# Optimization experiments

Measured on AMD Instinct MI355X. Metric: run time of the kernel, lower is better.

## Reference

```python
import jax, jax.numpy as jnp
import numpy as np

H = 8          # num_heads
D = 64         # head_dim
HID = 512      # hidden_size
W = 128        # window_size
NEG = -1e9

def setup_inputs() -> dict:
    key = jax.random.key(0)
    ks = jax.random.split(key, 12)
    B, S = 2, 2048
    def lin(i):
        w = jax.random.normal(ks[i], (HID, HID), dtype=jnp.float32) * (1.0 / np.sqrt(HID))
        b = jax.random.normal(ks[i + 1], (HID,), dtype=jnp.float32) * 0.01
        return w, b
    Wq, bq = lin(0)
    Wk, bk = lin(2)
    Wv, bv = lin(4)
    Wo, bo = lin(6)
    return {
        "value": jax.random.normal(ks[8], (B, S, HID), dtype=jnp.float32),
        "key": jax.random.normal(ks[9], (B, S, HID), dtype=jnp.float32),
        "query": jax.random.normal(ks[10], (B, S, HID), dtype=jnp.float32),
        "Wq": Wq, "bq": bq, "Wk": Wk, "bk": bk,
        "Wv": Wv, "bv": bv, "Wo": Wo, "bo": bo,
    }

def reference(value, key, query, Wq, bq, Wk, bk, Wv, bv, Wo, bo):
    B, S, _ = query.shape
    def heads(x, Wt, b):
        # torch Linear: x @ W.T + b ; then [B,S,H,D] -> [B,H,S,D]
        return (x @ Wt.T + b).reshape(B, S, H, D).transpose(0, 2, 1, 3)
    Q = heads(query, Wq, bq)
    K = heads(key, Wk, bk)
    V = heads(value, Wv, bv)
    scores = jnp.einsum('bhqd,bhkd->bhqk', Q, K) / jnp.sqrt(jnp.float32(D))
    idx = jnp.arange(S)
    local = jnp.abs(idx[:, None] - idx[None, :]) <= W  # [S,S] band mask
    scores = jnp.where(local[None, None], scores, NEG)
    weights = jax.nn.softmax(scores, axis=-1)
    out = jnp.einsum('bhqk,bhkd->bhqd', weights, V)
    out = out.transpose(0, 2, 1, 3).reshape(B, S, HID)
    return out @ Wo.T + bo
```

## Files before the change

kernel.cpp:

```cpp
#include <hip/hip_runtime.h>
#include <stdint.h>

#define B_   2
#define S_   2048
#define H_   8
#define D_   64
#define HID_ 512
#define W_   128
#define M_   (B_ * S_)
#define E_   (M_ * HID_)
#define WE_  (HID_ * HID_)
#define PPAD_ 72
#define M0_  12.0f

typedef unsigned short u16;
typedef __attribute__((ext_vector_type(8))) __bf16 bf16x8;
typedef __attribute__((ext_vector_type(4))) float  floatx4;

__device__ __forceinline__ float b2f(u16 u) {
    union { unsigned int i; float f; } x;
    x.i = ((unsigned int)u) << 16;
    return x.f;
}
__device__ __forceinline__ u16 f2b(float f) {
    union { float f; unsigned int i; } x;
    x.f = f;
    unsigned int r = x.i + 0x7FFFu + ((x.i >> 16) & 1u);
    return (u16)(r >> 16);
}

__device__ __forceinline__ void gll16(const u16* g, u16* l) {
    __builtin_amdgcn_global_load_lds(
        (const __attribute__((address_space(1))) unsigned int*)g,
        (__attribute__((address_space(3))) unsigned int*)l, 16, 0, 0);
}

__global__ __launch_bounds__(256) void split_kernel(
    const float* __restrict__ q, const float* __restrict__ k, const float* __restrict__ v,
    const float* __restrict__ wq, const float* __restrict__ wk,
    const float* __restrict__ wv, const float* __restrict__ wo,
    u16* __restrict__ U) {
    const int y = blockIdx.y;
    const float* src;
    u16* dst;
    int n;
    if (y < 3) {
        src = (y == 0) ? q : (y == 1) ? k : v;
        dst = U + (size_t)y * E_;
        n = E_;
    } else {
        src = (y == 3) ? wq : (y == 4) ? wk : (y == 5) ? wv : wo;
        dst = U + 3 * (size_t)E_ + (size_t)(y - 3) * WE_;
        n = WE_;
    }
    const int idx = (blockIdx.x * 256 + threadIdx.x) * 4;
    if (idx >= n) return;
    const float4 x = *(const float4*)(src + idx);
    ushort4 hs;
    hs.x = f2b(x.x); hs.y = f2b(x.y); hs.z = f2b(x.z); hs.w = f2b(x.w);
    *(ushort4*)(dst + idx) = hs;
}

template <int MODE, int PASSES, int BM, int BN>
__device__ __forceinline__ void gemm_mfma_body(
    const u16* __restrict__ Xh, const u16* __restrict__ Xl,
    const u16* __restrict__ Wh, const float* __restrict__ bias,
    float* __restrict__ outF, u16* __restrict__ outH) {
    constexpr int TM = BM / 64;
    constexpr int TN = BN / 16;
    constexpr int AGRP = BM / 16;
    constexpr int BGRP = BN / 16;

    __shared__ u16 As[2][PASSES][2][BM * 32];
    __shared__ u16 Bs[2][2][BN * 32];

    const int tid  = threadIdx.x;
    const int wave = tid >> 6;
    const int lane = tid & 63;
    const int r16  = lane & 15;
    const int quad = lane >> 4;
    const int srow = lane >> 2;
    const int sk   = (lane & 3) * 8;
    const int m0 = blockIdx.x * BM;
    const int n0 = blockIdx.y * BN;

    floatx4 zero = {0.f, 0.f, 0.f, 0.f};
    floatx4 acc[TM][TN];
#pragma unroll
    for (int i = 0; i < TM; i++)
#pragma unroll
        for (int j = 0; j < TN; j++) acc[i][j] = zero;

    auto stage = [&](int buf, int k0) {
        int slot = 0;
#pragma unroll
        for (int p = 0; p < PASSES; p++)
#pragma unroll
            for (int ks = 0; ks < 2; ks++)
#pragma unroll
                for (int g = 0; g < AGRP; g++, slot++)
                    if ((slot & 3) == wave) {
                        const u16* src = (p ? Xl : Xh) +
                            (size_t)(m0 + g * 16 + srow) * HID_ + k0 + ks * 32 + sk;
                        gll16(src, &As[buf][p][ks][g * 16 * 32]);
                    }
#pragma unroll
        for (int ks = 0; ks < 2; ks++)
#pragma unroll
            for (int g = 0; g < BGRP; g++, slot++)
                if ((slot & 3) == wave) {
                    const u16* src = Wh +
                        (size_t)(n0 + g * 16 + srow) * HID_ + k0 + ks * 32 + sk;
                    gll16(src, &Bs[buf][ks][g * 16 * 32]);
                }
    };

    stage(0, 0);
    constexpr int NIT = HID_ / 64;
    for (int it = 0; it < NIT; it++) {
        __syncthreads();
        if (it + 1 < NIT) stage((it + 1) & 1, (it + 1) * 64);
        const int buf = it & 1;

        bf16x8 bfr[2][TN];
#pragma unroll
        for (int ks = 0; ks < 2; ks++)
#pragma unroll
            for (int j = 0; j < TN; j++)
                bfr[ks][j] = *(const bf16x8*)&Bs[buf][ks][(j * 16 + r16) * 32 + quad * 8];
#pragma unroll
        for (int p = 0; p < PASSES; p++) {
            bf16x8 afr[2][TM];
#pragma unroll
            for (int ks = 0; ks < 2; ks++)
#pragma unroll
                for (int i = 0; i < TM; i++)
                    afr[ks][i] = *(const bf16x8*)
                        &As[buf][p][ks][(wave * TM * 16 + i * 16 + r16) * 32 + quad * 8];
#pragma unroll
            for (int ks = 0; ks < 2; ks++)
#pragma unroll
                for (int i = 0; i < TM; i++)
#pragma unroll
                    for (int j = 0; j < TN; j++)
                        acc[i][j] = __builtin_amdgcn_mfma_f32_16x16x32_bf16(
                            afr[ks][i], bfr[ks][j], acc[i][j], 0, 0, 0);
        }
    }

    const int m_base = m0 + wave * TM * 16;
    const int bb = m_base >> 11;
    if (MODE == 0) {
#pragma unroll
        for (int j = 0; j < TN; j++) {
            const int col = n0 + j * 16 + r16;
            const float bv = bias[col];
#pragma unroll
            for (int i = 0; i < TM; i++) {
                const int row0 = m_base + i * 16 + quad * 4;
#pragma unroll
                for (int r = 0; r < 4; r++)
                    outF[(size_t)(row0 + r) * HID_ + col] = acc[i][j][r] + bv;
            }
        }
    } else if (MODE == 1) {
#pragma unroll
        for (int j = 0; j < TN; j++) {
            const int col = n0 + j * 16 + r16;
            const int h = col >> 6, d = col & (D_ - 1);
            const float bv = bias[col];
            const size_t base = (size_t)(bb * H_ + h) * S_;
#pragma unroll
            for (int i = 0; i < TM; i++)
#pragma unroll
                for (int r = 0; r < 4; r++) {
                    const int s = (m_base & (S_ - 1)) + i * 16 + quad * 4 + r;
                    outH[(base + s) * D_ + d] = f2b(acc[i][j][r] + bv);
                }
        }
    } else {
#pragma unroll
        for (int j = 0; j < TN; j++) {
            const int col = n0 + j * 16 + r16;
            const int h = col >> 6, d = col & (D_ - 1);
            const float bv = bias[col];
            const size_t base = ((size_t)(bb * H_ + h) * D_ + d) * S_;
            const int s0 = (m_base & (S_ - 1)) + quad * 4;
#pragma unroll
            for (int i = 0; i < TM; i++) {
                ushort4 hs;
                hs.x = f2b(acc[i][j][0] + bv);
                hs.y = f2b(acc[i][j][1] + bv);
                hs.z = f2b(acc[i][j][2] + bv);
                hs.w = f2b(acc[i][j][3] + bv);
                *(ushort4*)(outH + base + s0 + i * 16) = hs;
            }
        }
    }
}

__global__ __launch_bounds__(256) void qkv_mfma_kernel(
    const u16* __restrict__ U,
    const float* __restrict__ bq, const float* __restrict__ bk, const float* __restrict__ bv,
    u16* __restrict__ P) {
    const u16* Wb = U + 3 * (size_t)E_;
    if (blockIdx.z == 0)
        gemm_mfma_body<1, 1, 128, 64>(U, nullptr, Wb, bq, nullptr, P);
    else if (blockIdx.z == 1)
        gemm_mfma_body<1, 1, 128, 64>(U + E_, nullptr, Wb + WE_, bk, nullptr, P + E_);
    else
        gemm_mfma_body<2, 1, 128, 64>(U + 2 * (size_t)E_, nullptr, Wb + 2 * WE_, bv,
                                      nullptr, P + 2 * (size_t)E_);
}

__global__ __launch_bounds__(256) void out_mfma_kernel(
    const u16* __restrict__ AOh, const u16* __restrict__ AOl,
    const u16* __restrict__ Woh, const float* __restrict__ bo,
    float* __restrict__ out) {
    gemm_mfma_body<0, 2, 64, 32>(AOh, AOl, Woh, bo, out, nullptr);
}

__global__ __launch_bounds__(256) void attn_kernel(
    const u16* __restrict__ Qh, const u16* __restrict__ Kh,
    const u16* __restrict__ Vth,
    u16* __restrict__ AOh, u16* __restrict__ AOl) {
    __shared__ u16   Ps[4][64][PPAD_];
    __shared__ float Ored[64][68];
    __shared__ float Lred[4][64];

    const int tid  = threadIdx.x;
    const int wave = tid >> 6;
    const int lane = tid & 63;
    const int r16 = lane & 15, quad = lane >> 4;
    const int qt = blockIdx.x, bh = blockIdx.y;
    const int q0 = qt * 64;
    const size_t sd = (size_t)bh * S_ * D_;
    const size_t ds = (size_t)bh * D_ * S_;

    floatx4 zero = {0.f, 0.f, 0.f, 0.f};
    floatx4 O[4][4];
    float lsum[4][4];
#pragma unroll
    for (int i = 0; i < 4; i++)
#pragma unroll
        for (int j = 0; j < 4; j++) O[i][j] = zero;
#pragma unroll
    for (int i = 0; i < 4; i++)
#pragma unroll
        for (int r = 0; r < 4; r++) lsum[i][r] = 0.f;

    int t_lo = qt - 2; if (t_lo < 0) t_lo = 0;
    int t_hi = qt + 2; if (t_hi > S_ / 64 - 1) t_hi = S_ / 64 - 1;

    for (int t = t_lo + wave; t <= t_hi; t += 4) {
        const int k0 = t * 64;
        floatx4 sa[4][4];
#pragma unroll
        for (int i = 0; i < 4; i++)
#pragma unroll
            for (int j = 0; j < 4; j++) sa[i][j] = zero;

#pragma unroll
        for (int ks = 0; ks < 2; ks++) {
            bf16x8 qf[4], kf[4];
#pragma unroll
            for (int i = 0; i < 4; i++)
                qf[i] = *(const bf16x8*)(Qh + sd + (size_t)(q0 + i * 16 + r16) * D_ + ks * 32 + quad * 8);
#pragma unroll
            for (int j = 0; j < 4; j++)
                kf[j] = *(const bf16x8*)(Kh + sd + (size_t)(k0 + j * 16 + r16) * D_ + ks * 32 + quad * 8);
#pragma unroll
            for (int i = 0; i < 4; i++)
#pragma unroll
                for (int j = 0; j < 4; j++)
                    sa[i][j] = __builtin_amdgcn_mfma_f32_16x16x32_bf16(qf[i], kf[j], sa[i][j], 0, 0, 0);
        }

#pragma unroll
        for (int i = 0; i < 4; i++)
#pragma unroll
            for (int j = 0; j < 4; j++) {
                const int kc = k0 + j * 16 + r16;
#pragma unroll
                for (int r = 0; r < 4; r++) {
                    const int q = q0 + i * 16 + quad * 4 + r;
                    const bool valid = (unsigned)(kc - q + W_) <= (unsigned)(2 * W_);
                    const float p = valid ? __expf(fmaf(sa[i][j][r], 0.125f, -M0_)) : 0.f;
                    lsum[i][r] += p;
                    Ps[wave][i * 16 + quad * 4 + r][j * 16 + r16] = f2b(p);
                }
            }

#pragma unroll
        for (int ks = 0; ks < 2; ks++) {
            bf16x8 pf[4], vf[4];
#pragma unroll
            for (int i = 0; i < 4; i++)
                pf[i] = *(const bf16x8*)&Ps[wave][i * 16 + r16][ks * 32 + quad * 8];
#pragma unroll
            for (int j = 0; j < 4; j++)
                vf[j] = *(const bf16x8*)(Vth + ds + (size_t)(j * 16 + r16) * S_ + k0 + ks * 32 + quad * 8);
#pragma unroll
            for (int i = 0; i < 4; i++)
#pragma unroll
                for (int j = 0; j < 4; j++)
                    O[i][j] = __builtin_amdgcn_mfma_f32_16x16x32_bf16(pf[i], vf[j], O[i][j], 0, 0, 0);
        }
    }

#pragma unroll
    for (int i = 0; i < 4; i++)
#pragma unroll
        for (int r = 0; r < 4; r++) {
            float l = lsum[i][r];
#pragma unroll
            for (int off = 1; off < 16; off <<= 1) l += __shfl_xor(l, off, 64);
            if (r16 == 0) Lred[wave][i * 16 + quad * 4 + r] = l;
        }

    const bool active = (t_lo + wave <= t_hi);
#pragma unroll
    for (int w = 0; w < 4; w++) {
        if (wave == w && active) {
#pragma unroll
            for (int i = 0; i < 4; i++)
#pragma unroll
                for (int j = 0; j < 4; j++) {
                    floatx4* cell = (floatx4*)&Ored[j * 16 + r16][i * 16 + quad * 4];
                    if (w == 0) *cell = O[i][j];
                    else        *cell = *cell + O[i][j];
                }
        }
        __syncthreads();
    }

    const int b = bh >> 3, h = bh & 7;
    const int q  = tid >> 2;
    const int d0 = (tid & 3) * 16;
    const float linv = 1.f / (Lred[0][q] + Lred[1][q] + Lred[2][q] + Lred[3][q]);
    const size_t base = (size_t)(b * S_ + q0 + q) * HID_ + h * D_ + d0;
#pragma unroll
    for (int k = 0; k < 16; k++) {
        const float v = Ored[d0 + k][q] * linv;
        const u16 hh = f2b(v);
        AOh[base + k] = hh;
        AOl[base + k] = f2b(v - b2f(hh));
    }
}

extern "C" void kernel_launch(void* const* d_in, const int* in_sizes, int n_in,
                              void* d_out, int out_size, void* d_ws, size_t ws_size,
                              hipStream_t stream) {
    const float* value = (const float*)d_in[0];
    const float* key_  = (const float*)d_in[1];
    const float* query = (const float*)d_in[2];
    const float* bq = (const float*)d_in[4];
    const float* bk = (const float*)d_in[6];
    const float* bv = (const float*)d_in[8];
    const float* bo = (const float*)d_in[10];

    u16* U = (u16*)d_ws;
    u16* P = U + 3 * (size_t)E_ + 4 * (size_t)WE_;
    u16* AOh = U;
    u16* AOl = U + E_;
    const u16* Wb = U + 3 * (size_t)E_;

    split_kernel<<<dim3(E_ / 1024, 7), 256, 0, stream>>>(
        query, key_, value,
        (const float*)d_in[3], (const float*)d_in[5],
        (const float*)d_in[7], (const float*)d_in[9], U);
    qkv_mfma_kernel<<<dim3(M_ / 128, HID_ / 64, 3), 256, 0, stream>>>(
        U, bq, bk, bv, P);
    attn_kernel<<<dim3(S_ / 64, B_ * H_), 256, 0, stream>>>(
        P, P + E_, P + 2 * (size_t)E_, AOh, AOl);
    out_mfma_kernel<<<dim3(M_ / 64, HID_ / 32), 256, 0, stream>>>(
        AOh, AOl, Wb + 3 * WE_, bo, (float*)d_out);
}
```

Measured before the change: 155.2 us.

## Fuse all stages into one persistent kernel with software grid barriers

Replaces the four separate launches (convert, QKV GEMM, attention, output GEMM) with one persistent kernel of 512 blocks. Stages are separated by atomic-counter grid barriers, and shared memory is aliased across stages. The aim is to remove launch gaps and inter-kernel drain between stages. The output GEMM tile also changes from 64x32 to 64x64. This relies on all 512 blocks being co-resident. The barrier-reset scheme (CAS on a sentinel, resets of later cells) is fragile, and the spin-waits add overhead.

New measurement: 498.3 us. 3.21x slower.

```diff
diff --git a/kernel.cpp b/kernel.cpp
--- a/kernel.cpp
+++ b/kernel.cpp
@@ -12,6 +12,7 @@
 #define WE_  (HID_ * HID_)
 #define PPAD_ 72
 #define M0_  12.0f
+#define NB_  512
 
 typedef unsigned short u16;
 typedef __attribute__((ext_vector_type(8))) __bf16 bf16x8;
@@ -35,44 +36,55 @@
         (__attribute__((address_space(3))) unsigned int*)l, 16, 0, 0);
 }
 
-__global__ __launch_bounds__(256) void split_kernel(
-    const float* __restrict__ q, const float* __restrict__ k, const float* __restrict__ v,
-    const float* __restrict__ wq, const float* __restrict__ wk,
-    const float* __restrict__ wv, const float* __restrict__ wo,
-    u16* __restrict__ U) {
-    const int y = blockIdx.y;
-    const float* src;
-    u16* dst;
-    int n;
-    if (y < 3) {
-        src = (y == 0) ? q : (y == 1) ? k : v;
-        dst = U + (size_t)y * E_;
-        n = E_;
-    } else {
-        src = (y == 3) ? wq : (y == 4) ? wk : (y == 5) ? wv : wo;
-        dst = U + 3 * (size_t)E_ + (size_t)(y - 3) * WE_;
-        n = WE_;
-    }
-    const int idx = (blockIdx.x * 256 + threadIdx.x) * 4;
-    if (idx >= n) return;
-    const float4 x = *(const float4*)(src + idx);
-    ushort4 hs;
-    hs.x = f2b(x.x); hs.y = f2b(x.y); hs.z = f2b(x.z); hs.w = f2b(x.w);
-    *(ushort4*)(dst + idx) = hs;
+__device__ __forceinline__ void grid_barrier(unsigned* cells, int idx) {
+    __threadfence();
+    __syncthreads();
+    if (threadIdx.x == 0) {
+        unsigned* c = cells + idx * 32;
+        if (idx == 0) {
+            atomicCAS(c, 0xAAAAAAAAu, 0u);
+            if (blockIdx.x == 0) {
+                atomicExch(cells + 32, 0u);
+                atomicExch(cells + 64, 0u);
+            }
+        }
+        atomicAdd(c, 1u);
+        long cap = 0;
+        while (__hip_atomic_load(c, __ATOMIC_RELAXED, __HIP_MEMORY_SCOPE_AGENT)
+                   < (unsigned)NB_ && ++cap < 200000000L)
+            __builtin_amdgcn_s_sleep(2);
+    }
+    __syncthreads();
+    __threadfence();
+}
+
+__device__ __forceinline__ void cvt_tensor(const float* __restrict__ src,
+                                           u16* __restrict__ dst, int n4) {
+    const int T = gridDim.x * blockDim.x;
+    for (int i = blockIdx.x * blockDim.x + threadIdx.x; i < n4; i += T) {
+        const float4 x = ((const float4*)src)[i];
+        ushort4 h;
+        h.x = f2b(x.x); h.y = f2b(x.y); h.z = f2b(x.z); h.w = f2b(x.w);
+        ((ushort4*)dst)[i] = h;
+    }
 }
 
 template <int MODE, int PASSES, int BM, int BN>
-__device__ __forceinline__ void gemm_mfma_body(
+__device__ __forceinline__ void gemm_job(char* smem,
     const u16* __restrict__ Xh, const u16* __restrict__ Xl,
     const u16* __restrict__ Wh, const float* __restrict__ bias,
-    float* __restrict__ outF, u16* __restrict__ outH) {
+    float* __restrict__ outF, u16* __restrict__ outH, int bx, int by) {
     constexpr int TM = BM / 64;
     constexpr int TN = BN / 16;
-    constexpr int AGRP = BM / 16;
-    constexpr int BGRP = BN / 16;
-
-    __shared__ u16 As[2][PASSES][2][BM * 32];
-    __shared__ u16 Bs[2][2][BN * 32];
+    constexpr int AS_KS  = BM * 32;
+    constexpr int AS_P   = 2 * AS_KS;
+    constexpr int AS_BUF = PASSES * AS_P;
+    constexpr int ATOT   = 2 * AS_BUF;
+    constexpr int BS_KS  = BN * 32;
+    constexpr int BS_BUF = 2 * BS_KS;
+
+    u16* SA = (u16*)smem;
+    u16* SB = SA + ATOT;
 
     const int tid  = threadIdx.x;
     const int wave = tid >> 6;
@@ -81,8 +93,8 @@
     const int quad = lane >> 4;
     const int srow = lane >> 2;
     const int sk   = (lane & 3) * 8;
-    const int m0 = blockIdx.x * BM;
-    const int n0 = blockIdx.y * BN;
+    const int m0 = bx * BM;
+    const int n0 = by * BN;
 
     floatx4 zero = {0.f, 0.f, 0.f, 0.f};
     floatx4 acc[TM][TN];
@@ -98,20 +110,20 @@
 #pragma unroll
             for (int ks = 0; ks < 2; ks++)
 #pragma unroll
-                for (int g = 0; g < AGRP; g++, slot++)
+                for (int g = 0; g < BM / 16; g++, slot++)
                     if ((slot & 3) == wave) {
                         const u16* src = (p ? Xl : Xh) +
                             (size_t)(m0 + g * 16 + srow) * HID_ + k0 + ks * 32 + sk;
-                        gll16(src, &As[buf][p][ks][g * 16 * 32]);
+                        gll16(src, &SA[buf * AS_BUF + p * AS_P + ks * AS_KS + g * 16 * 32]);
                     }
 #pragma unroll
         for (int ks = 0; ks < 2; ks++)
 #pragma unroll
-            for (int g = 0; g < BGRP; g++, slot++)
+            for (int g = 0; g < BN / 16; g++, slot++)
                 if ((slot & 3) == wave) {
                     const u16* src = Wh +
                         (size_t)(n0 + g * 16 + srow) * HID_ + k0 + ks * 32 + sk;
-                    gll16(src, &Bs[buf][ks][g * 16 * 32]);
+                    gll16(src, &SB[buf * BS_BUF + ks * BS_KS + g * 16 * 32]);
                 }
     };
 
@@ -127,7 +139,8 @@
         for (int ks = 0; ks < 2; ks++)
 #pragma unroll
             for (int j = 0; j < TN; j++)
-                bfr[ks][j] = *(const bf16x8*)&Bs[buf][ks][(j * 16 + r16) * 32 + quad * 8];
+                bfr[ks][j] = *(const bf16x8*)
+                    &SB[buf * BS_BUF + ks * BS_KS + (j * 16 + r16) * 32 + quad * 8];
 #pragma unroll
         for (int p = 0; p < PASSES; p++) {
             bf16x8 afr[2][TM];
@@ -136,7 +149,8 @@
 #pragma unroll
                 for (int i = 0; i < TM; i++)
                     afr[ks][i] = *(const bf16x8*)
-                        &As[buf][p][ks][(wave * TM * 16 + i * 16 + r16) * 32 + quad * 8];
+                        &SA[buf * AS_BUF + p * AS_P + ks * AS_KS +
+                            (wave * TM * 16 + i * 16 + r16) * 32 + quad * 8];
 #pragma unroll
             for (int ks = 0; ks < 2; ks++)
 #pragma unroll
@@ -147,6 +161,7 @@
                             afr[ks][i], bfr[ks][j], acc[i][j], 0, 0, 0);
         }
     }
+    __syncthreads();
 
     const int m_base = m0 + wave * TM * 16;
     const int bb = m_base >> 11;
@@ -199,40 +214,17 @@
     }
 }
 
-__global__ __launch_bounds__(256) void qkv_mfma_kernel(
-    const u16* __restrict__ U,
-    const float* __restrict__ bq, const float* __restrict__ bk, const float* __restrict__ bv,
-    u16* __restrict__ P) {
-    const u16* Wb = U + 3 * (size_t)E_;
-    if (blockIdx.z == 0)
-        gemm_mfma_body<1, 1, 128, 64>(U, nullptr, Wb, bq, nullptr, P);
-    else if (blockIdx.z == 1)
-        gemm_mfma_body<1, 1, 128, 64>(U + E_, nullptr, Wb + WE_, bk, nullptr, P + E_);
-    else
-        gemm_mfma_body<2, 1, 128, 64>(U + 2 * (size_t)E_, nullptr, Wb + 2 * WE_, bv,
-                                      nullptr, P + 2 * (size_t)E_);
-}
-
-__global__ __launch_bounds__(256) void out_mfma_kernel(
-    const u16* __restrict__ AOh, const u16* __restrict__ AOl,
-    const u16* __restrict__ Woh, const float* __restrict__ bo,
-    float* __restrict__ out) {
-    gemm_mfma_body<0, 2, 64, 32>(AOh, AOl, Woh, bo, out, nullptr);
-}
-
-__global__ __launch_bounds__(256) void attn_kernel(
+__device__ __forceinline__ void attn_job(char* smem,
     const u16* __restrict__ Qh, const u16* __restrict__ Kh,
     const u16* __restrict__ Vth,
-    u16* __restrict__ AOh, u16* __restrict__ AOl) {
-    __shared__ u16   Ps[4][64][PPAD_];
-    __shared__ float Ored[64][68];
-    __shared__ float Lred[4][64];
+    u16* __restrict__ AOh, u16* __restrict__ AOl, int qt, int bh) {
+    u16 (*Ps)[64][PPAD_] = (u16(*)[64][PPAD_])smem;
+    float* Lred = (float*)(smem + 4 * 64 * PPAD_ * 2);
 
     const int tid  = threadIdx.x;
     const int wave = tid >> 6;
     const int lane = tid & 63;
     const int r16 = lane & 15, quad = lane >> 4;
-    const int qt = blockIdx.x, bh = blockIdx.y;
     const int q0 = qt * 64;
     const size_t sd = (size_t)bh * S_ * D_;
     const size_t ds = (size_t)bh * D_ * S_;
@@ -315,9 +307,12 @@
             float l = lsum[i][r];
 #pragma unroll
             for (int off = 1; off < 16; off <<= 1) l += __shfl_xor(l, off, 64);
-            if (r16 == 0) Lred[wave][i * 16 + quad * 4 + r] = l;
-        }
-
+            if (r16 == 0) Lred[wave * 64 + i * 16 + quad * 4 + r] = l;
+        }
+
+    __syncthreads();
+
+    float (*Ored)[68] = (float(*)[68])smem;
     const bool active = (t_lo + wave <= t_hi);
 #pragma unroll
     for (int w = 0; w < 4; w++) {
@@ -337,7 +332,7 @@
     const int b = bh >> 3, h = bh & 7;
     const int q  = tid >> 2;
     const int d0 = (tid & 3) * 16;
-    const float linv = 1.f / (Lred[0][q] + Lred[1][q] + Lred[2][q] + Lred[3][q]);
+    const float linv = 1.f / (Lred[q] + Lred[64 + q] + Lred[128 + q] + Lred[192 + q]);
     const size_t base = (size_t)(b * S_ + q0 + q) * HID_ + h * D_ + d0;
 #pragma unroll
     for (int k = 0; k < 16; k++) {
@@ -345,6 +340,56 @@
         const u16 hh = f2b(v);
         AOh[base + k] = hh;
         AOl[base + k] = f2b(v - b2f(hh));
+    }
+    __syncthreads();
+}
+
+__global__ __launch_bounds__(256, 2) void fused_kernel(
+    const float* __restrict__ xv, const float* __restrict__ xk, const float* __restrict__ xq,
+    const float* __restrict__ wq, const float* __restrict__ bq,
+    const float* __restrict__ wk, const float* __restrict__ bk,
+    const float* __restrict__ wv, const float* __restrict__ bv,
+    const float* __restrict__ wo, const float* __restrict__ bo,
+    u16* __restrict__ U, unsigned* __restrict__ bar, float* __restrict__ out) {
+    __shared__ char smem[49152];
+
+    u16* P   = U + 3 * (size_t)E_ + 4 * (size_t)WE_;
+    u16* AOh = U;
+    u16* AOl = U + E_;
+    const u16* Wb = U + 3 * (size_t)E_;
+
+    cvt_tensor(xq, U,            E_ / 4);
+    cvt_tensor(xk, U + E_,       E_ / 4);
+    cvt_tensor(xv, U + 2 * (size_t)E_, E_ / 4);
+    cvt_tensor(wq, (u16*)Wb,           WE_ / 4);
+    cvt_tensor(wk, (u16*)Wb + WE_,     WE_ / 4);
+    cvt_tensor(wv, (u16*)Wb + 2 * WE_, WE_ / 4);
+    cvt_tensor(wo, (u16*)Wb + 3 * WE_, WE_ / 4);
+    grid_barrier(bar, 0);
+
+    for (int j = blockIdx.x; j < 768; j += gridDim.x) {
+        const int mat = j >> 8, t = j & 255, bx = t >> 3, by = t & 7;
+        if (mat == 0)
+            gemm_job<1, 1, 128, 64>(smem, U, nullptr, Wb, bq, nullptr, P, bx, by);
+        else if (mat == 1)
+            gemm_job<1, 1, 128, 64>(smem, U + E_, nullptr, Wb + WE_, bk,
+                                    nullptr, P + E_, bx, by);
+        else
+            gemm_job<2, 1, 128, 64>(smem, U + 2 * (size_t)E_, nullptr, Wb + 2 * WE_, bv,
+                                    nullptr, P + 2 * (size_t)E_, bx, by);
+    }
+    grid_barrier(bar, 1);
+
+    {
+        const int j = blockIdx.x;
+        attn_job(smem, P, P + E_, P + 2 * (size_t)E_, AOh, AOl, j & 31, j >> 5);
+    }
+    grid_barrier(bar, 2);
+
+    {
+        const int j = blockIdx.x;
+        gemm_job<0, 2, 64, 64>(smem, AOh, AOl, Wb + 3 * WE_, bo, out, nullptr,
+                               j >> 3, j & 7);
     }
 }
 
@@ -354,25 +399,15 @@
     const float* value = (const float*)d_in[0];
     const float* key_  = (const float*)d_in[1];
     const float* query = (const float*)d_in[2];
-    const float* bq = (const float*)d_in[4];
-    const float* bk = (const float*)d_in[6];
-    const float* bv = (const float*)d_in[8];
-    const float* bo = (const float*)d_in[10];
 
     u16* U = (u16*)d_ws;
-    u16* P = U + 3 * (size_t)E_ + 4 * (size_t)WE_;
-    u16* AOh = U;
-    u16* AOl = U + E_;
-    const u16* Wb = U + 3 * (size_t)E_;
-
-    split_kernel<<<dim3(E_ / 1024, 7), 256, 0, stream>>>(
-        query, key_, value,
-        (const float*)d_in[3], (const float*)d_in[5],
-        (const float*)d_in[7], (const float*)d_in[9], U);
-    qkv_mfma_kernel<<<dim3(M_ / 128, HID_ / 64, 3), 256, 0, stream>>>(
-        U, bq, bk, bv, P);
-    attn_kernel<<<dim3(S_ / 64, B_ * H_), 256, 0, stream>>>(
-        P, P + E_, P + 2 * (size_t)E_, AOh, AOl);
-    out_mfma_kernel<<<dim3(M_ / 64, HID_ / 32), 256, 0, stream>>>(
-        AOh, AOl, Wb + 3 * WE_, bo, (float*)d_out);
-}
+    unsigned* bar = (unsigned*)((char*)d_ws + (40u << 20));
+
+    fused_kernel<<<dim3(NB_), dim3(256), 0, stream>>>(
+        value, key_, query,
+        (const float*)d_in[3], (const float*)d_in[4],
+        (const float*)d_in[5], (const float*)d_in[6],
+        (const float*)d_in[7], (const float*)d_in[8],
+        (const float*)d_in[9], (const float*)d_in[10],
+        U, bar, (float*)d_out);
+}
```
